# Performance work log

Hardware: AMD Instinct MI355X
Metric: run time of the kernel (lower is better)

## Reference

```python
import jax, jax.numpy as jnp
import numpy as np

B, D, L, H = 2048, 64, 64, 512  # batch, in_dim, latent_space, hidden


def setup_inputs() -> dict:
    key = jax.random.key(0)
    ks = jax.random.split(key, 12)
    inp = {
        "x": jax.random.normal(ks[0], (B, D), jnp.float32),
        "koopman": jax.random.normal(ks[1], (B, L, D), jnp.float32),
    }
    dims = [(L, H), (H, H), (H, H), (H, D)]
    k = 2
    for pfx in ("s", "t"):
        for j, (fi, fo) in enumerate(dims):
            inp[f"{pfx}W{j+1}"] = jax.random.normal(ks[k], (fi, fo), jnp.float32) / np.sqrt(fi).astype(np.float32)
            inp[f"{pfx}b{j+1}"] = jnp.zeros((fo,), jnp.float32)
            k += 1
    return inp


def _mlp(z, W1, b1, W2, b2, W3, b3, W4, b4):
    h = jnp.tanh(z @ W1 + b1)
    h = jnp.tanh(h @ W2 + b2)
    h = jnp.tanh(h @ W3 + b3)
    return h @ W4 + b4


def reference(x, koopman,
              sW1, sb1, sW2, sb2, sW3, sb3, sW4, sb4,
              tW1, tb1, tW2, tb2, tW3, tb3, tW4, tb4):
    # koopman: (B, L, D) -> z: (B, D, L); column i of the torch loop is z[:, i, :]
    z = jnp.swapaxes(koopman, 1, 2)
    s = _mlp(z, sW1, sb1, sW2, sb2, sW3, sb3, sW4, sb4)  # (B, D, D)
    t = _mlp(z, tW1, tb1, tW2, tb2, tW3, tb3, tW4, tb4)  # (B, D, D)
    # loop kept only output column i for input column i -> diagonal over last two dims
    ds = jnp.diagonal(s, axis1=1, axis2=2)  # (B, D)
    dt = jnp.diagonal(t, axis1=1, axis2=2)  # (B, D)
    return (x - dt) * jnp.exp(-ds)
```

## Files before the change

kernel.cpp:

```cpp
#include <hip/hip_runtime.h>


typedef _Float16 f16;
typedef _Float16 f16x8 __attribute__((ext_vector_type(8)));
typedef float f32x4 __attribute__((ext_vector_type(4)));

#define WPACK_PER_NET 589824
#define OFF_W1 0
#define OFF_W2 32768
#define OFF_W3 294912
#define OFF_W4T 557056
#define WPACK_BYTES (2u * WPACK_PER_NET * sizeof(f16))

__device__ __forceinline__ void lds_barrier() {
  asm volatile("s_waitcnt lgkmcnt(0)\n\ts_barrier" ::: "memory");
}

__global__ void pack_weights(const float* __restrict__ sW1, const float* __restrict__ sW2,
                             const float* __restrict__ sW3, const float* __restrict__ sW4,
                             const float* __restrict__ tW1, const float* __restrict__ tW2,
                             const float* __restrict__ tW3, const float* __restrict__ tW4,
                             f16* __restrict__ dst) {
  int idx = blockIdx.x * 256 + threadIdx.x;
  int net = idx >= WPACK_PER_NET;
  int f = idx - net * WPACK_PER_NET;
  const float* W;
  int base;
  if (f < OFF_W2) {
    W = net ? tW1 : sW1; base = OFF_W1;
  } else if (f < OFF_W3) {
    W = net ? tW2 : sW2; base = OFF_W2;
  } else if (f < OFF_W4T) {
    W = net ? tW3 : sW3; base = OFF_W3;
  } else {
    int f4 = f - OFF_W4T;
    dst[idx] = (f16)((net ? tW4 : sW4)[(f4 & 511) * 64 + (f4 >> 9)]);
    return;
  }
  int fl = f - base;
  int j = fl & 7, ln = (fl >> 3) & 63, nt = (fl >> 9) & 3, w = (fl >> 11) & 7,
      kk = fl >> 14;
  dst[idx] =
      (f16)W[(kk * 32 + (ln >> 4) * 8 + j) * 512 + w * 64 + nt * 16 + (ln & 15)];
}

__device__ __forceinline__ int aidx(int m, int k) {
  return (((k >> 5) * 4 + (m >> 4)) * 64 + (m & 15) + ((k >> 3) & 3) * 16) * 8 + (k & 7);
}

__device__ __forceinline__ float fast_tanh(float x) {
  float e = __expf(x + x);
  return fmaf(-2.0f, __builtin_amdgcn_rcpf(e + 1.0f), 1.0f);
}

template <int NS>
__device__ __forceinline__ void mlp_layer(const char* __restrict__ wlb,
                                          const float* __restrict__ bias,
                                          const f16* Asrc, f16* Hout,
                                          int wave, int lane, int sbase) {
  f32x4 acc[4][4];
#pragma unroll
  for (int nt = 0; nt < 4; nt++) {
    float bv = bias[wave * 64 + nt * 16 + (lane & 15)];
#pragma unroll
    for (int mt = 0; mt < 4; mt++) acc[mt][nt] = f32x4{bv, bv, bv, bv};
  }
  f16x8 bb[2][4];
#pragma unroll
  for (int nt = 0; nt < 4; nt++) bb[0][nt] = *(const f16x8*)(wlb + nt * 1024);
#pragma unroll
  for (int kk = 0; kk < NS; kk++) {
    if (kk + 1 < NS) {
      const char* q = wlb + (kk + 1) * 32768;
#pragma unroll
      for (int nt = 0; nt < 4; nt++)
        bb[(kk + 1) & 1][nt] = *(const f16x8*)(q + nt * 1024);
    }
    const f16* ab = Asrc + kk * 2048 + lane * 8;
#pragma unroll
    for (int mt = 0; mt < 4; mt++) {
      f16x8 a = *(const f16x8*)(ab + mt * 512);
#pragma unroll
      for (int nt = 0; nt < 4; nt++)
        acc[mt][nt] = __builtin_amdgcn_mfma_f32_16x16x32_f16(a, bb[kk & 1][nt],
                                                             acc[mt][nt], 0, 0, 0);
    }
  }
  lds_barrier();
  f16* hb = Hout + sbase;
#pragma unroll
  for (int mt = 0; mt < 4; mt++)
#pragma unroll
    for (int nt = 0; nt < 4; nt++)
#pragma unroll
      for (int r = 0; r < 4; r++)
        hb[(nt >> 1) * 2048 + mt * 512 + (nt & 1) * 256 + r * 8] =
            (f16)fast_tanh(acc[mt][nt][r]);
  lds_barrier();
}

__global__ __launch_bounds__(512, 4) void decoder_main(
    const float* __restrict__ x, const float* __restrict__ koop,
    const f16* __restrict__ wpack,
    const float* __restrict__ sb1, const float* __restrict__ sb2,
    const float* __restrict__ sb3, const float* __restrict__ sb4,
    const float* __restrict__ tb1, const float* __restrict__ tb2,
    const float* __restrict__ tb3, const float* __restrict__ tb4,
    float* __restrict__ out) {
  __shared__ __align__(16) f16 ZA[4096];
  __shared__ __align__(16) f16 HA[32768];
  __shared__ float redBuf[2][64];

  const int b = blockIdx.x;
  const int t = threadIdx.x;
  const int wave = t >> 6, lane = t & 63;
  const int sbase =
      wave * 4096 + (lane >> 4) * 32 + ((lane & 15) >> 3) * 128 + (lane & 7);
  const char* wbb = (const char*)wpack + wave * 4096 + lane * 16;

  const float* kb = koop + b * 4096;
#pragma unroll
  for (int i = 0; i < 8; i++) {
    int flat = t + 512 * i;
    ZA[aidx(flat & 63, flat >> 6)] = (f16)kb[flat];
  }
  lds_barrier();

  for (int net = 0; net < 2; net++) {
    const size_t nb = (size_t)net * (WPACK_PER_NET * 2);
    const float* b1 = net ? tb1 : sb1;
    const float* b2 = net ? tb2 : sb2;
    const float* b3 = net ? tb3 : sb3;
    const float* b4 = net ? tb4 : sb4;
    mlp_layer<2>(wbb + nb + OFF_W1 * 2, b1, ZA, HA, wave, lane, sbase);
    mlp_layer<16>(wbb + nb + OFF_W2 * 2, b2, HA, HA, wave, lane, sbase);
    mlp_layer<16>(wbb + nb + OFF_W3 * 2, b3, HA, HA, wave, lane, sbase);

    const f16* w4t = wpack + net * WPACK_PER_NET + OFF_W4T;
    int i = t >> 3, sub = t & 7;
    float p = 0.f;
#pragma unroll
    for (int q = 0; q < 8; q++) {
      int k0 = sub * 64 + q * 8;
      f16x8 hv = *(const f16x8*)&HA[aidx(i, k0)];
      f16x8 wv = *(const f16x8*)&w4t[i * 512 + k0];
#pragma unroll
      for (int j = 0; j < 8; j++) p += (float)hv[j] * (float)wv[j];
    }
    p += __shfl_down(p, 4, 8);
    p += __shfl_down(p, 2, 8);
    p += __shfl_down(p, 1, 8);
    if (sub == 0) redBuf[net][i] = p + b4[i];
    lds_barrier();
  }

  if (t < 64) {
    out[b * 64 + t] = (x[b * 64 + t] - redBuf[1][t]) * __expf(-redBuf[0][t]);
  }
}

__device__ __forceinline__ void load_b_direct(const float* __restrict__ Wraw,
                                              int kk, int wave, int lane,
                                              f16x8* bdst) {
  int n0 = wave * 64 + (lane & 15);
  int kb = kk * 32 + (lane >> 4) * 8;
#pragma unroll
  for (int nt = 0; nt < 4; nt++) {
    f16x8 v;
#pragma unroll
    for (int j = 0; j < 8; j++) v[j] = (f16)Wraw[(kb + j) * 512 + n0 + nt * 16];
    bdst[nt] = v;
  }
}

template <int NS>
__device__ __forceinline__ void mlp_layer_direct(
    const float* __restrict__ Wraw, const float* __restrict__ bias,
    const f16* Asrc, f16* Hout, int wave, int lane, int sbase) {
  f32x4 acc[4][4];
#pragma unroll
  for (int nt = 0; nt < 4; nt++) {
    float bv = bias[wave * 64 + nt * 16 + (lane & 15)];
#pragma unroll
    for (int mt = 0; mt < 4; mt++) acc[mt][nt] = f32x4{bv, bv, bv, bv};
  }
  f16x8 bb[2][4];
  load_b_direct(Wraw, 0, wave, lane, bb[0]);
#pragma unroll
  for (int kk = 0; kk < NS; kk++) {
    if (kk + 1 < NS) load_b_direct(Wraw, kk + 1, wave, lane, bb[(kk + 1) & 1]);
    const f16* ab = Asrc + kk * 2048 + lane * 8;
#pragma unroll
    for (int mt = 0; mt < 4; mt++) {
      f16x8 a = *(const f16x8*)(ab + mt * 512);
#pragma unroll
      for (int nt = 0; nt < 4; nt++)
        acc[mt][nt] = __builtin_amdgcn_mfma_f32_16x16x32_f16(a, bb[kk & 1][nt],
                                                             acc[mt][nt], 0, 0, 0);
    }
  }
  __syncthreads();
  f16* hb = Hout + sbase;
#pragma unroll
  for (int mt = 0; mt < 4; mt++)
#pragma unroll
    for (int nt = 0; nt < 4; nt++)
#pragma unroll
      for (int r = 0; r < 4; r++)
        hb[(nt >> 1) * 2048 + mt * 512 + (nt & 1) * 256 + r * 8] =
            (f16)fast_tanh(acc[mt][nt][r]);
  __syncthreads();
}

__global__ __launch_bounds__(512, 4) void decoder_direct(
    const float* __restrict__ x, const float* __restrict__ koop,
    const float* __restrict__ sW1, const float* __restrict__ sW2,
    const float* __restrict__ sW3, const float* __restrict__ sW4,
    const float* __restrict__ tW1, const float* __restrict__ tW2,
    const float* __restrict__ tW3, const float* __restrict__ tW4,
    const float* __restrict__ sb1, const float* __restrict__ sb2,
    const float* __restrict__ sb3, const float* __restrict__ sb4,
    const float* __restrict__ tb1, const float* __restrict__ tb2,
    const float* __restrict__ tb3, const float* __restrict__ tb4,
    float* __restrict__ out) {
  __shared__ __align__(16) f16 ZA[4096];
  __shared__ __align__(16) f16 HA[32768];
  __shared__ float redBuf[2][64];
  const int b = blockIdx.x;
  const int t = threadIdx.x;
  const int wave = t >> 6, lane = t & 63;
  const int sbase =
      wave * 4096 + (lane >> 4) * 32 + ((lane & 15) >> 3) * 128 + (lane & 7);
  const float* kb = koop + b * 4096;
#pragma unroll
  for (int i = 0; i < 8; i++) {
    int flat = t + 512 * i;
    ZA[aidx(flat & 63, flat >> 6)] = (f16)kb[flat];
  }
  __syncthreads();
  for (int net = 0; net < 2; net++) {
    const float* W1 = net ? tW1 : sW1;
    const float* W2 = net ? tW2 : sW2;
    const float* W3 = net ? tW3 : sW3;
    const float* W4 = net ? tW4 : sW4;
    const float* b1 = net ? tb1 : sb1;
    const float* b2 = net ? tb2 : sb2;
    const float* b3 = net ? tb3 : sb3;
    const float* b4 = net ? tb4 : sb4;
    mlp_layer_direct<2>(W1, b1, ZA, HA, wave, lane, sbase);
    mlp_layer_direct<16>(W2, b2, HA, HA, wave, lane, sbase);
    mlp_layer_direct<16>(W3, b3, HA, HA, wave, lane, sbase);
    int i = t >> 3, sub = t & 7;
    float p = 0.f;
#pragma unroll
    for (int q = 0; q < 8; q++) {
      int k0 = sub * 64 + q * 8;
      f16x8 hv = *(const f16x8*)&HA[aidx(i, k0)];
#pragma unroll
      for (int j = 0; j < 8; j++) p += (float)hv[j] * W4[(k0 + j) * 64 + i];
    }
    p += __shfl_down(p, 4, 8);
    p += __shfl_down(p, 2, 8);
    p += __shfl_down(p, 1, 8);
    if (sub == 0) redBuf[net][i] = p + b4[i];
    __syncthreads();
  }
  if (t < 64) {
    out[b * 64 + t] = (x[b * 64 + t] - redBuf[1][t]) * __expf(-redBuf[0][t]);
  }
}

extern "C" void kernel_launch(void* const* d_in, const int* in_sizes, int n_in,
                              void* d_out, int out_size, void* d_ws, size_t ws_size,
                              hipStream_t stream) {
  const float* x    = (const float*)d_in[0];
  const float* koop = (const float*)d_in[1];
  const float* sW1 = (const float*)d_in[2];  const float* sb1 = (const float*)d_in[3];
  const float* sW2 = (const float*)d_in[4];  const float* sb2 = (const float*)d_in[5];
  const float* sW3 = (const float*)d_in[6];  const float* sb3 = (const float*)d_in[7];
  const float* sW4 = (const float*)d_in[8];  const float* sb4 = (const float*)d_in[9];
  const float* tW1 = (const float*)d_in[10]; const float* tb1 = (const float*)d_in[11];
  const float* tW2 = (const float*)d_in[12]; const float* tb2 = (const float*)d_in[13];
  const float* tW3 = (const float*)d_in[14]; const float* tb3 = (const float*)d_in[15];
  const float* tW4 = (const float*)d_in[16]; const float* tb4 = (const float*)d_in[17];
  float* out = (float*)d_out;

  if (ws_size >= (size_t)WPACK_BYTES) {
    f16* wpack = (f16*)d_ws;
    pack_weights<<<4608, 256, 0, stream>>>(sW1, sW2, sW3, sW4, tW1, tW2, tW3, tW4,
                                           wpack);
    decoder_main<<<2048, 512, 0, stream>>>(x, koop, wpack,
                                           sb1, sb2, sb3, sb4,
                                           tb1, tb2, tb3, tb4, out);
  } else {
    decoder_direct<<<2048, 512, 0, stream>>>(
        x, koop, sW1, sW2, sW3, sW4, tW1, tW2, tW3, tW4,
        sb1, sb2, sb3, sb4, tb1, tb2, tb3, tb4, out);
  }
}
```

Before: 439.9 us.

## Use 32x32x16 MFMA and process two batch items per block

Each block now handles two batch samples (128 rows of M) instead of one, so every weight tile loaded from global memory is reused across twice as many rows. The per-wave tile is built from 32x32x16 MFMA instructions with a matching repacked weight and activation LDS layout, which cuts B-operand loads per FLOP. LDS use doubles to about 147KB and the launch bound drops to 2 blocks per CU, lowering occupancy. The grid is halved to 1024 blocks.

```diff
diff --git a/kernel.cpp b/kernel.cpp
--- a/kernel.cpp
+++ b/kernel.cpp
@@ -3,7 +3,7 @@
 
 typedef _Float16 f16;
 typedef _Float16 f16x8 __attribute__((ext_vector_type(8)));
-typedef float f32x4 __attribute__((ext_vector_type(4)));
+typedef float f32x16 __attribute__((ext_vector_type(16)));
 
 #define WPACK_PER_NET 589824
 #define OFF_W1 0
@@ -38,14 +38,13 @@
     return;
   }
   int fl = f - base;
-  int j = fl & 7, ln = (fl >> 3) & 63, nt = (fl >> 9) & 3, w = (fl >> 11) & 7,
-      kk = fl >> 14;
-  dst[idx] =
-      (f16)W[(kk * 32 + (ln >> 4) * 8 + j) * 512 + w * 64 + nt * 16 + (ln & 15)];
-}
-
-__device__ __forceinline__ int aidx(int m, int k) {
-  return (((k >> 5) * 4 + (m >> 4)) * 64 + (m & 15) + ((k >> 3) & 3) * 16) * 8 + (k & 7);
+  int j = fl & 7, ln = (fl >> 3) & 63, nt = (fl >> 9) & 1, w = (fl >> 10) & 7,
+      s = fl >> 13;
+  dst[idx] = (f16)W[(s * 16 + (ln >> 5) * 8 + j) * 512 + w * 64 + nt * 32 + (ln & 31)];
+}
+
+__device__ __forceinline__ int aidx2(int m, int k) {
+  return (((k >> 4) * 4 + (m >> 5)) * 64 + (m & 31) + ((k >> 3) & 1) * 32) * 8 + (k & 7);
 }
 
 __device__ __forceinline__ float fast_tanh(float x) {
@@ -53,37 +52,41 @@
   return fmaf(-2.0f, __builtin_amdgcn_rcpf(e + 1.0f), 1.0f);
 }
 
-template <int NS>
+template <int NS2>
 __device__ __forceinline__ void mlp_layer(const char* __restrict__ wlb,
                                           const float* __restrict__ bias,
                                           const f16* Asrc, f16* Hout,
                                           int wave, int lane, int sbase) {
-  f32x4 acc[4][4];
-#pragma unroll
-  for (int nt = 0; nt < 4; nt++) {
-    float bv = bias[wave * 64 + nt * 16 + (lane & 15)];
-#pragma unroll
-    for (int mt = 0; mt < 4; mt++) acc[mt][nt] = f32x4{bv, bv, bv, bv};
-  }
-  f16x8 bb[2][4];
-#pragma unroll
-  for (int nt = 0; nt < 4; nt++) bb[0][nt] = *(const f16x8*)(wlb + nt * 1024);
-#pragma unroll
-  for (int kk = 0; kk < NS; kk++) {
-    if (kk + 1 < NS) {
-      const char* q = wlb + (kk + 1) * 32768;
-#pragma unroll
-      for (int nt = 0; nt < 4; nt++)
-        bb[(kk + 1) & 1][nt] = *(const f16x8*)(q + nt * 1024);
-    }
-    const f16* ab = Asrc + kk * 2048 + lane * 8;
+  f32x16 acc[4][2];
+  {
+    float bv0 = bias[wave * 64 + (lane & 31)];
+    float bv1 = bias[wave * 64 + 32 + (lane & 31)];
+#pragma unroll
+    for (int mt = 0; mt < 4; mt++)
+#pragma unroll
+      for (int r = 0; r < 16; r++) {
+        acc[mt][0][r] = bv0;
+        acc[mt][1][r] = bv1;
+      }
+  }
+  f16x8 bb[2][2];
+  bb[0][0] = *(const f16x8*)(wlb);
+  bb[0][1] = *(const f16x8*)(wlb + 1024);
+#pragma unroll
+  for (int s = 0; s < NS2; s++) {
+    if (s + 1 < NS2) {
+      const char* q = wlb + (s + 1) * 16384;
+      bb[(s + 1) & 1][0] = *(const f16x8*)(q);
+      bb[(s + 1) & 1][1] = *(const f16x8*)(q + 1024);
+    }
+    const f16* ab = Asrc + s * 2048 + lane * 8;
 #pragma unroll
     for (int mt = 0; mt < 4; mt++) {
       f16x8 a = *(const f16x8*)(ab + mt * 512);
-#pragma unroll
-      for (int nt = 0; nt < 4; nt++)
-        acc[mt][nt] = __builtin_amdgcn_mfma_f32_16x16x32_f16(a, bb[kk & 1][nt],
-                                                             acc[mt][nt], 0, 0, 0);
+      acc[mt][0] = __builtin_amdgcn_mfma_f32_32x32x16_f16(a, bb[s & 1][0],
+                                                          acc[mt][0], 0, 0, 0);
+      acc[mt][1] = __builtin_amdgcn_mfma_f32_32x32x16_f16(a, bb[s & 1][1],
+                                                          acc[mt][1], 0, 0, 0);
     }
   }
   lds_barrier();
@@ -91,15 +94,15 @@
 #pragma unroll
   for (int mt = 0; mt < 4; mt++)
 #pragma unroll
-    for (int nt = 0; nt < 4; nt++)
-#pragma unroll
-      for (int r = 0; r < 4; r++)
-        hb[(nt >> 1) * 2048 + mt * 512 + (nt & 1) * 256 + r * 8] =
+    for (int nt = 0; nt < 2; nt++)
+#pragma unroll
+      for (int r = 0; r < 16; r++)
+        hb[nt * 4096 + mt * 512 + (r >> 2) * 64 + (r & 3) * 8] =
             (f16)fast_tanh(acc[mt][nt][r]);
   lds_barrier();
 }
 
-__global__ __launch_bounds__(512, 4) void decoder_main(
+__global__ __launch_bounds__(512, 2) void decoder_main(
     const float* __restrict__ x, const float* __restrict__ koop,
     const f16* __restrict__ wpack,
     const float* __restrict__ sb1, const float* __restrict__ sb2,
@@ -107,22 +110,24 @@
     const float* __restrict__ tb1, const float* __restrict__ tb2,
     const float* __restrict__ tb3, const float* __restrict__ tb4,
     float* __restrict__ out) {
-  __shared__ __align__(16) f16 ZA[4096];
-  __shared__ __align__(16) f16 HA[32768];
-  __shared__ float redBuf[2][64];
+  __shared__ __align__(16) f16 ZA[8192];
+  __shared__ __align__(16) f16 HA[65536];
+  __shared__ float redBuf[2][128];
 
   const int b = blockIdx.x;
   const int t = threadIdx.x;
   const int wave = t >> 6, lane = t & 63;
-  const int sbase =
-      wave * 4096 + (lane >> 4) * 32 + ((lane & 15) >> 3) * 128 + (lane & 7);
-  const char* wbb = (const char*)wpack + wave * 4096 + lane * 16;
-
-  const float* kb = koop + b * 4096;
-#pragma unroll
-  for (int i = 0; i < 8; i++) {
+  const int ln5 = lane & 31, q5 = lane >> 5;
+  const int sbase = wave * 8192 + (ln5 >> 4) * 2048 + ((ln5 >> 3) & 1) * 256 +
+                    q5 * 32 + (ln5 & 7);
+  const char* wbb = (const char*)wpack + wave * 2048 + lane * 16;
+
+  const float* kb = koop + (size_t)b * 8192;
+#pragma unroll
+  for (int i = 0; i < 16; i++) {
     int flat = t + 512 * i;
-    ZA[aidx(flat & 63, flat >> 6)] = (f16)kb[flat];
+    int bi = flat >> 12, rem = flat & 4095;
+    ZA[aidx2(bi * 64 + (rem & 63), rem >> 6)] = (f16)kb[flat];
   }
   lds_barrier();
 
@@ -132,31 +137,36 @@
     const float* b2 = net ? tb2 : sb2;
     const float* b3 = net ? tb3 : sb3;
     const float* b4 = net ? tb4 : sb4;
-    mlp_layer<2>(wbb + nb + OFF_W1 * 2, b1, ZA, HA, wave, lane, sbase);
-    mlp_layer<16>(wbb + nb + OFF_W2 * 2, b2, HA, HA, wave, lane, sbase);
-    mlp_layer<16>(wbb + nb + OFF_W3 * 2, b3, HA, HA, wave, lane, sbase);
+    mlp_layer<4>(wbb + nb + OFF_W1 * 2, b1, ZA, HA, wave, lane, sbase);
+    mlp_layer<32>(wbb + nb + OFF_W2 * 2, b2, HA, HA, wave, lane, sbase);
+    mlp_layer<32>(wbb + nb + OFF_W3 * 2, b3, HA, HA, wave, lane, sbase);
 
     const f16* w4t = wpack + net * WPACK_PER_NET + OFF_W4T;
-    int i = t >> 3, sub = t & 7;
+    int i2 = t >> 2, sub = t & 3;
     float p = 0.f;
 #pragma unroll
-    for (int q = 0; q < 8; q++) {
-      int k0 = sub * 64 + q * 8;
-      f16x8 hv = *(const f16x8*)&HA[aidx(i, k0)];
-      f16x8 wv = *(const f16x8*)&w4t[i * 512 + k0];
+    for (int qq = 0; qq < 16; qq++) {
+      int k0 = sub * 128 + qq * 8;
+      f16x8 hv = *(const f16x8*)&HA[aidx2(i2, k0)];
+      f16x8 wv = *(const f16x8*)&w4t[(i2 & 63) * 512 + k0];
 #pragma unroll
       for (int j = 0; j < 8; j++) p += (float)hv[j] * (float)wv[j];
     }
-    p += __shfl_down(p, 4, 8);
-    p += __shfl_down(p, 2, 8);
-    p += __shfl_down(p, 1, 8);
-    if (sub == 0) redBuf[net][i] = p + b4[i];
+    p += __shfl_down(p, 2, 4);
+    p += __shfl_down(p, 1, 4);
+    if (sub == 0) redBuf[net][i2] = p + b4[i2 & 63];
     lds_barrier();
   }
 
-  if (t < 64) {
-    out[b * 64 + t] = (x[b * 64 + t] - redBuf[1][t]) * __expf(-redBuf[0][t]);
-  }
+  if (t < 128) {
+    out[b * 128 + t] = (x[b * 128 + t] - redBuf[1][t]) * __expf(-redBuf[0][t]);
+  }
+}
+
+typedef float f32x4 __attribute__((ext_vector_type(4)));
+
+__device__ __forceinline__ int aidx(int m, int k) {
+  return (((k >> 5) * 4 + (m >> 4)) * 64 + (m & 15) + ((k >> 3) & 3) * 16) * 8 + (k & 7);
 }
 
 __device__ __forceinline__ void load_b_direct(const float* __restrict__ Wraw,
@@ -253,8 +263,8 @@
     int i = t >> 3, sub = t & 7;
     float p = 0.f;
 #pragma unroll
-    for (int q = 0; q < 8; q++) {
-      int k0 = sub * 64 + q * 8;
+    for (int qq = 0; qq < 8; qq++) {
+      int k0 = sub * 64 + qq * 8;
       f16x8 hv = *(const f16x8*)&HA[aidx(i, k0)];
 #pragma unroll
       for (int j = 0; j < 8; j++) p += (float)hv[j] * W4[(k0 + j) * 64 + i];
@@ -289,7 +299,7 @@
     f16* wpack = (f16*)d_ws;
     pack_weights<<<4608, 256, 0, stream>>>(sW1, sW2, sW3, sW4, tW1, tW2, tW3, tW4,
                                            wpack);
-    decoder_main<<<2048, 512, 0, stream>>>(x, koop, wpack,
+    decoder_main<<<1024, 512, 0, stream>>>(x, koop, wpack,
                                            sb1, sb2, sb3, sb4,
                                            tb1, tb2, tb3, tb4, out);
   } else {
```

After: 460.0 us. 1.05x slower.
